# Performance work log

Hardware: AMD Instinct MI355X
Metric: run time of the kernel (lower is better)

The kernel has to match this reference:

```python
import jax, jax.numpy as jnp
import numpy as np

NEG_INF = -1e6  # d2l masked_softmax fill value


def setup_inputs() -> dict:
    key = jax.random.key(0)
    kq, kk, kv, kl = jax.random.split(key, 4)
    n, s, d = 32, 2048, 64
    queries = jax.random.normal(kq, (n, s, d), dtype=jnp.float32)
    keys = jax.random.normal(kk, (n, s, d), dtype=jnp.float32)
    values = jax.random.normal(kv, (n, s, d), dtype=jnp.float32)
    valid_lens = jax.random.randint(kl, (n,), 1, s + 1, dtype=jnp.int32)
    return {"queries": queries, "keys": keys, "values": values, "valid_lens": valid_lens}


def reference(queries, keys, values, valid_lens):
    d = queries.shape[-1]
    # scores: [n, q, k]
    scores = jnp.einsum("nqd,nkd->nqk", queries, keys) / jnp.sqrt(jnp.float32(d))
    kv_len = scores.shape[-1]
    # masked_softmax: positions >= valid_len get NEG_INF before softmax
    mask = jnp.arange(kv_len, dtype=jnp.int32)[None, None, :] < valid_lens[:, None, None]
    scores = jnp.where(mask, scores, NEG_INF)
    attn = jax.nn.softmax(scores, axis=-1)
    # dropout rate 0.0 (inference) -> identity
    return jnp.einsum("nqk,nkd->nqd", attn, values)
```

## Files before the change

### kernel.cpp

```cpp
#include <hip/hip_runtime.h>
#include <hip/hip_bf16.h>


typedef short bf16x8 __attribute__((ext_vector_type(8)));
typedef float f32x4  __attribute__((ext_vector_type(4)));
typedef float f32x16 __attribute__((ext_vector_type(16)));
typedef unsigned int u32;
typedef u32 u32x4 __attribute__((ext_vector_type(4)));

#define SEQ 2048
#define DH 64
#define BK 64
#define LDSP 72
#define FRAG 512
#define TILE_SH 4096
#define SCLQ 0.18033688011112042f

static __device__ __forceinline__ short f2bf(float f) {
    unsigned u = __float_as_uint(f);
    return (short)((u + 0x7FFFu + ((u >> 16) & 1u)) >> 16);
}
static __device__ __forceinline__ u32 pk2bf(float lo, float hi) {
    __hip_bfloat162 h = __float22bfloat162_rn(float2{lo, hi});
    return *(u32*)&h;
}
static __device__ __forceinline__ void pl32swap(u32& a, u32& b) {
    asm volatile("v_permlane32_swap_b32 %0, %1" : "+v"(a), "+v"(b));
}

__global__ __launch_bounds__(256, 4)
void prepass(const float* __restrict__ K, const float* __restrict__ V,
             short* __restrict__ KF, short* __restrict__ VF)
{
    __shared__ short T[DH][LDSP];

    const int tid  = threadIdx.x;
    const int wave = tid >> 6;
    const int lane = tid & 63;
    const int b  = blockIdx.x & 31;
    const int t  = blockIdx.x >> 5;
    const int k0 = t * BK;
    const size_t bo = (size_t)b * SEQ * DH;
    const size_t tb = (size_t)(b * 32 + t) * TILE_SH;

    const float* Ks = K + bo + (size_t)k0 * DH;
    short* Kd = KF + tb;
    #pragma unroll
    for (int h = 0; h < 2; ++h) {
        const int c = tid + h * 256;
        const int f = c >> 6;
        const int row = (f & 1) * 32 + (c & 31);
        const int col = (f >> 1) * 16 + ((c >> 5) & 1) * 8;
        f32x4 a = *(const f32x4*)(Ks + row * DH + col);
        f32x4 d = *(const f32x4*)(Ks + row * DH + col + 4);
        u32x4 o;
        o[0] = pk2bf(a[0], a[1]); o[1] = pk2bf(a[2], a[3]);
        o[2] = pk2bf(d[0], d[1]); o[3] = pk2bf(d[2], d[3]);
        *(u32x4*)(Kd + c * 8) = o;
    }

    #pragma unroll
    for (int h = 0; h < 2; ++h) {
        const int d0 = wave * 8 + h * 32;
        const float* src = V + bo + (size_t)(k0 + lane) * DH + d0;
        f32x4 va = *(const f32x4*)(src);
        f32x4 vb = *(const f32x4*)(src + 4);
        #pragma unroll
        for (int j = 0; j < 4; ++j) {
            T[d0 + j][lane]     = f2bf(va[j]);
            T[d0 + 4 + j][lane] = f2bf(vb[j]);
        }
    }
    __syncthreads();

    short* Vd = VF + tb;
    #pragma unroll
    for (int h = 0; h < 2; ++h) {
        const int c = tid + h * 256;
        const int f = c >> 6;
        const int trow = (f & 1) * 32 + (c & 31);
        const int tcol = (f >> 1) * 16 + ((c >> 5) & 1) * 8;
        *(bf16x8*)(Vd + c * 8) = *(const bf16x8*)(&T[trow][tcol]);
    }
}

template <bool PRE>
__global__ __launch_bounds__(256, 4)
void attn_fwd(const float* __restrict__ Q,
              const float* __restrict__ Kf, const float* __restrict__ Vf,
              const short* __restrict__ KF, const short* __restrict__ VF,
              const int* __restrict__ VL, float* __restrict__ O)
{
    __shared__ __align__(16) float Red[2][64][44];
    __shared__ int Rsort[32];

    const int tid  = threadIdx.x;
    const int wave = tid >> 6;
    const int lane = tid & 63;
    const int qg   = wave & 1;
    const int pg   = wave >> 1;
    const int hi   = lane >> 5;
    const int l31  = lane & 31;

    if (tid < 32) {
        const int nv = (VL[tid] + BK - 1) >> 6;
        int rank = 0;
        for (int jj = 0; jj < 32; ++jj) {
            const int nj = (VL[jj] + BK - 1) >> 6;
            rank += (nj > nv) || (nj == nv && jj < tid);
        }
        Rsort[rank] = tid;
    }
    __syncthreads();

    const int jb = blockIdx.x & 255;
    const int sl = blockIdx.x >> 8;
    const int c8 = jb >> 5;
    const int qt = jb & 31;
    const int rk = (sl == 0) ? c8 : (sl == 1) ? (15 - c8)
                 : (sl == 2) ? (16 + c8) : (31 - c8);
    int b = Rsort[rk];
    b = __builtin_amdgcn_readfirstlane(b);

    const int vl  = __builtin_amdgcn_readfirstlane(VL[b]);
    const int nkt = (vl + BK - 1) >> 6;

    const size_t bo = (size_t)b * SEQ * DH;
    const short* KFb = KF + (size_t)b * 32 * TILE_SH;
    const short* VFb = VF + (size_t)b * 32 * TILE_SH;
    const float* Kf32 = Kf + bo;
    const float* Vf32 = Vf + bo;

    const int qrow = qt * 64 + qg * 32 + l31;
    bf16x8 aq[4];
    {
        const float* qp = Q + bo + (size_t)qrow * DH + hi * 8;
        #pragma unroll
        for (int st = 0; st < 4; ++st) {
            f32x4 a = *(const f32x4*)(qp + st * 16);
            f32x4 c = *(const f32x4*)(qp + st * 16 + 4);
            #pragma unroll
            for (int j = 0; j < 4; ++j) {
                aq[st][j]     = f2bf(a[j] * SCLQ);
                aq[st][j + 4] = f2bf(c[j] * SCLQ);
            }
        }
    }

    f32x16 oacc0, oacc1;
    #pragma unroll
    for (int i = 0; i < 16; ++i) { oacc0[i] = 0.f; oacc1[i] = 0.f; }
    float Lrun = 0.f;

    const int lo8 = lane * 8;

    for (int kt = pg; kt < nkt; kt += 2) {
        const int k0 = kt * BK;
        const short* kf = KFb + (size_t)kt * TILE_SH;
        const short* vf = VFb + (size_t)kt * TILE_SH;

        auto ldA = [&](int f) -> bf16x8 {
            if constexpr (PRE) {
                return *(const bf16x8*)(kf + f * FRAG + lo8);
            } else {
                const int st = f >> 1, kh = f & 1;
                const float* p = Kf32 + (size_t)(k0 + kh * 32 + l31) * DH + st * 16 + hi * 8;
                f32x4 x = *(const f32x4*)p;
                f32x4 y = *(const f32x4*)(p + 4);
                bf16x8 r;
                #pragma unroll
                for (int j = 0; j < 4; ++j) { r[j] = f2bf(x[j]); r[j + 4] = f2bf(y[j]); }
                return r;
            }
        };
        auto ldV = [&](int f) -> bf16x8 {
            if constexpr (PRE) {
                return *(const bf16x8*)(vf + f * FRAG + lo8);
            } else {
                const int ks = f >> 1, dh = f & 1;
                bf16x8 r;
                #pragma unroll
                for (int j = 0; j < 8; ++j)
                    r[j] = f2bf(Vf32[(size_t)(k0 + ks * 16 + hi * 8 + j) * DH + dh * 32 + l31]);
                return r;
            }
        };

        f32x16 s0, s1;
        #pragma unroll
        for (int i = 0; i < 16; ++i) { s0[i] = 0.f; s1[i] = 0.f; }

        __builtin_amdgcn_s_setprio(1);
        bf16x8 A00 = ldA(0), A01 = ldA(1);
        bf16x8 A10 = ldA(2), A11 = ldA(3);
        s0 = __builtin_amdgcn_mfma_f32_32x32x16_bf16(A00, aq[0], s0, 0, 0, 0);
        s1 = __builtin_amdgcn_mfma_f32_32x32x16_bf16(A01, aq[0], s1, 0, 0, 0);
        bf16x8 A20 = ldA(4), A21 = ldA(5);
        s0 = __builtin_amdgcn_mfma_f32_32x32x16_bf16(A10, aq[1], s0, 0, 0, 0);
        s1 = __builtin_amdgcn_mfma_f32_32x32x16_bf16(A11, aq[1], s1, 0, 0, 0);
        bf16x8 A30 = ldA(6), A31 = ldA(7);
        s0 = __builtin_amdgcn_mfma_f32_32x32x16_bf16(A20, aq[2], s0, 0, 0, 0);
        s1 = __builtin_amdgcn_mfma_f32_32x32x16_bf16(A21, aq[2], s1, 0, 0, 0);
        s0 = __builtin_amdgcn_mfma_f32_32x32x16_bf16(A30, aq[3], s0, 0, 0, 0);
        s1 = __builtin_amdgcn_mfma_f32_32x32x16_bf16(A31, aq[3], s1, 0, 0, 0);
        __builtin_amdgcn_s_setprio(0);

        bf16x8 V00 = ldV(0), V01 = ldV(1);
        bf16x8 V10 = ldV(2), V11 = ldV(3);

        if (k0 + BK <= vl) {
            #pragma unroll
            for (int r = 0; r < 16; ++r) {
                s0[r] = __builtin_amdgcn_exp2f(s0[r]);
                s1[r] = __builtin_amdgcn_exp2f(s1[r]);
            }
        } else {
            #pragma unroll
            for (int r = 0; r < 16; ++r) {
                const int krow = k0 + (r & 3) + 8 * (r >> 2) + 4 * hi;
                s0[r] = (krow < vl)      ? __builtin_amdgcn_exp2f(s0[r]) : 0.f;
                s1[r] = (krow + 32 < vl) ? __builtin_amdgcn_exp2f(s1[r]) : 0.f;
            }
        }

        {
            float ls = 0.f;
            #pragma unroll
            for (int r = 0; r < 16; ++r) ls += s0[r] + s1[r];
            u32 a = __float_as_uint(ls), c = a;
            pl32swap(a, c);
            Lrun += __uint_as_float(a) + __uint_as_float(c);
        }

        u32 pk0[8], pk1[8];
        #pragma unroll
        for (int i = 0; i < 8; ++i) {
            pk0[i] = pk2bf(s0[2 * i], s0[2 * i + 1]);
            pk1[i] = pk2bf(s1[2 * i], s1[2 * i + 1]);
        }
        bf16x8 ap[4];
        #pragma unroll
        for (int t = 0; t < 2; ++t) {
            u32 x0 = pk0[4 * t], x1 = pk0[4 * t + 1];
            u32 x2 = pk0[4 * t + 2], x3 = pk0[4 * t + 3];
            pl32swap(x0, x2); pl32swap(x1, x3);
            u32x4 w; w[0] = x0; w[1] = x1; w[2] = x2; w[3] = x3;
            ap[t] = *(bf16x8*)&w;
            u32 y0 = pk1[4 * t], y1 = pk1[4 * t + 1];
            u32 y2 = pk1[4 * t + 2], y3 = pk1[4 * t + 3];
            pl32swap(y0, y2); pl32swap(y1, y3);
            u32x4 v; v[0] = y0; v[1] = y1; v[2] = y2; v[3] = y3;
            ap[2 + t] = *(bf16x8*)&v;
        }

        __builtin_amdgcn_s_setprio(1);
        oacc0 = __builtin_amdgcn_mfma_f32_32x32x16_bf16(ap[0], V00, oacc0, 0, 0, 0);
        oacc1 = __builtin_amdgcn_mfma_f32_32x32x16_bf16(ap[0], V01, oacc1, 0, 0, 0);
        bf16x8 V20 = ldV(4), V21 = ldV(5);
        oacc0 = __builtin_amdgcn_mfma_f32_32x32x16_bf16(ap[1], V10, oacc0, 0, 0, 0);
        oacc1 = __builtin_amdgcn_mfma_f32_32x32x16_bf16(ap[1], V11, oacc1, 0, 0, 0);
        bf16x8 V30 = ldV(6), V31 = ldV(7);
        oacc0 = __builtin_amdgcn_mfma_f32_32x32x16_bf16(ap[2], V20, oacc0, 0, 0, 0);
        oacc1 = __builtin_amdgcn_mfma_f32_32x32x16_bf16(ap[2], V21, oacc1, 0, 0, 0);
        oacc0 = __builtin_amdgcn_mfma_f32_32x32x16_bf16(ap[3], V30, oacc0, 0, 0, 0);
        oacc1 = __builtin_amdgcn_mfma_f32_32x32x16_bf16(ap[3], V31, oacc1, 0, 0, 0);
        __builtin_amdgcn_s_setprio(0);
    }

    float* rp = &Red[qg][lane][0];
    if (pg == 1) {
        #pragma unroll
        for (int wd = 0; wd < 4; ++wd) {
            f32x4 t0, t1;
            #pragma unroll
            for (int i = 0; i < 4; ++i) { t0[i] = oacc0[wd * 4 + i]; t1[i] = oacc1[wd * 4 + i]; }
            *(f32x4*)(rp + wd * 4)      = t0;
            *(f32x4*)(rp + 16 + wd * 4) = t1;
        }
        rp[32] = Lrun;
    }
    __syncthreads();
    if (pg == 0) {
        f32x4 p0[4], p1[4];
        #pragma unroll
        for (int wd = 0; wd < 4; ++wd) {
            p0[wd] = *(const f32x4*)(rp + wd * 4);
            p1[wd] = *(const f32x4*)(rp + 16 + wd * 4);
        }
        const float Lq = Lrun + rp[32];
        #pragma unroll
        for (int r = 0; r < 16; ++r) {
            const int rb = (r & 3) + 8 * (r >> 2) + 4 * hi;
            const float inv = 1.0f / __shfl(Lq, rb);
            const int row = qt * 64 + qg * 32 + rb;
            O[bo + (size_t)row * DH + l31]      = (oacc0[r] + p0[r >> 2][r & 3]) * inv;
            O[bo + (size_t)row * DH + 32 + l31] = (oacc1[r] + p1[r >> 2][r & 3]) * inv;
        }
    }
}

extern "C" void kernel_launch(void* const* d_in, const int* in_sizes, int n_in,
                              void* d_out, int out_size, void* d_ws, size_t ws_size,
                              hipStream_t stream) {
    const float* Q  = (const float*)d_in[0];
    const float* K  = (const float*)d_in[1];
    const float* V  = (const float*)d_in[2];
    const int*   VL = (const int*)d_in[3];
    float* O = (float*)d_out;

    const size_t nel = (size_t)32 * 32 * TILE_SH;
    const size_t need = 2 * nel * sizeof(short);
    if (ws_size >= need) {
        short* KF = (short*)d_ws;
        short* VF = KF + nel;
        prepass<<<dim3(1024), dim3(256), 0, stream>>>(K, V, KF, VF);
        attn_fwd<true><<<dim3(1024), dim3(256), 0, stream>>>(Q, K, V, KF, VF, VL, O);
    } else {
        attn_fwd<false><<<dim3(1024), dim3(256), 0, stream>>>(Q, K, V, nullptr, nullptr, VL, O);
    }
}
```

Baseline: 134.7 us.

## Split key tiles across four waves per 32-row query block with tree reduction

Each block now handles 32 query rows instead of 64, and all four waves stride over key tiles by four, so the grid doubles to 2048 blocks. Partial outputs and row sums are combined through a two-stage LDS tree reduction with an extra barrier. Block ordering becomes simple batch-rank-major, dropping the previous serpentine interleave. The aim is more parallelism and shorter per-wave key loops for the uneven valid lengths, at the cost of re-reading K/V tiles from twice as many blocks and extra reduction synchronisation.

```diff
diff --git a/kernel.cpp b/kernel.cpp
--- a/kernel.cpp
+++ b/kernel.cpp
@@ -14,6 +14,7 @@
 #define LDSP 72
 #define FRAG 512
 #define TILE_SH 4096
+#define PSTRIDE 36
 #define SCLQ 0.18033688011112042f
 
 static __device__ __forceinline__ short f2bf(float f) {
@@ -91,14 +92,12 @@
               const short* __restrict__ KF, const short* __restrict__ VF,
               const int* __restrict__ VL, float* __restrict__ O)
 {
-    __shared__ __align__(16) float Red[2][64][44];
+    __shared__ __align__(16) float Red[2][64][PSTRIDE];
     __shared__ int Rsort[32];
 
     const int tid  = threadIdx.x;
     const int wave = tid >> 6;
     const int lane = tid & 63;
-    const int qg   = wave & 1;
-    const int pg   = wave >> 1;
     const int hi   = lane >> 5;
     const int l31  = lane & 31;
 
@@ -113,12 +112,8 @@
     }
     __syncthreads();
 
-    const int jb = blockIdx.x & 255;
-    const int sl = blockIdx.x >> 8;
-    const int c8 = jb >> 5;
-    const int qt = jb & 31;
-    const int rk = (sl == 0) ? c8 : (sl == 1) ? (15 - c8)
-                 : (sl == 2) ? (16 + c8) : (31 - c8);
+    const int qq = blockIdx.x & 63;
+    const int rk = blockIdx.x >> 6;
     int b = Rsort[rk];
     b = __builtin_amdgcn_readfirstlane(b);
 
@@ -131,7 +126,7 @@
     const float* Kf32 = Kf + bo;
     const float* Vf32 = Vf + bo;
 
-    const int qrow = qt * 64 + qg * 32 + l31;
+    const int qrow = qq * 32 + l31;
     bf16x8 aq[4];
     {
         const float* qp = Q + bo + (size_t)qrow * DH + hi * 8;
@@ -154,7 +149,7 @@
 
     const int lo8 = lane * 8;
 
-    for (int kt = pg; kt < nkt; kt += 2) {
+    for (int kt = wave; kt < nkt; kt += 4) {
         const int k0 = kt * BK;
         const short* kf = KFb + (size_t)kt * TILE_SH;
         const short* vf = VFb + (size_t)kt * TILE_SH;
@@ -167,10 +162,10 @@
                 const float* p = Kf32 + (size_t)(k0 + kh * 32 + l31) * DH + st * 16 + hi * 8;
                 f32x4 x = *(const f32x4*)p;
                 f32x4 y = *(const f32x4*)(p + 4);
-                bf16x8 r;
+                bf16x8 rr;
                 #pragma unroll
-                for (int j = 0; j < 4; ++j) { r[j] = f2bf(x[j]); r[j + 4] = f2bf(y[j]); }
-                return r;
+                for (int j = 0; j < 4; ++j) { rr[j] = f2bf(x[j]); rr[j + 4] = f2bf(y[j]); }
+                return rr;
             }
         };
         auto ldV = [&](int f) -> bf16x8 {
@@ -178,11 +173,11 @@
                 return *(const bf16x8*)(vf + f * FRAG + lo8);
             } else {
                 const int ks = f >> 1, dh = f & 1;
-                bf16x8 r;
+                bf16x8 rr;
                 #pragma unroll
                 for (int j = 0; j < 8; ++j)
-                    r[j] = f2bf(Vf32[(size_t)(k0 + ks * 16 + hi * 8 + j) * DH + dh * 32 + l31]);
-                return r;
+                    rr[j] = f2bf(Vf32[(size_t)(k0 + ks * 16 + hi * 8 + j) * DH + dh * 32 + l31]);
+                return rr;
             }
         };
 
@@ -267,8 +262,8 @@
         __builtin_amdgcn_s_setprio(0);
     }
 
-    float* rp = &Red[qg][lane][0];
-    if (pg == 1) {
+    if (wave & 1) {
+        float* rp = &Red[wave >> 1][lane][0];
         #pragma unroll
         for (int wd = 0; wd < 4; ++wd) {
             f32x4 t0, t1;
@@ -280,21 +275,48 @@
         rp[32] = Lrun;
     }
     __syncthreads();
-    if (pg == 0) {
-        f32x4 p0[4], p1[4];
+    if (!(wave & 1)) {
+        const float* rp = &Red[wave >> 1][lane][0];
         #pragma unroll
         for (int wd = 0; wd < 4; ++wd) {
-            p0[wd] = *(const f32x4*)(rp + wd * 4);
-            p1[wd] = *(const f32x4*)(rp + 16 + wd * 4);
+            f32x4 t0 = *(const f32x4*)(rp + wd * 4);
+            f32x4 t1 = *(const f32x4*)(rp + 16 + wd * 4);
+            #pragma unroll
+            for (int i = 0; i < 4; ++i) { oacc0[wd * 4 + i] += t0[i]; oacc1[wd * 4 + i] += t1[i]; }
+        }
+        Lrun += rp[32];
+    }
+    __syncthreads();
+    if (wave == 2) {
+        float* rp = &Red[0][lane][0];
+        #pragma unroll
+        for (int wd = 0; wd < 4; ++wd) {
+            f32x4 t0, t1;
+            #pragma unroll
+            for (int i = 0; i < 4; ++i) { t0[i] = oacc0[wd * 4 + i]; t1[i] = oacc1[wd * 4 + i]; }
+            *(f32x4*)(rp + wd * 4)      = t0;
+            *(f32x4*)(rp + 16 + wd * 4) = t1;
+        }
+        rp[32] = Lrun;
+    }
+    __syncthreads();
+    if (wave == 0) {
+        const float* rp = &Red[0][lane][0];
+        #pragma unroll
+        for (int wd = 0; wd < 4; ++wd) {
+            f32x4 t0 = *(const f32x4*)(rp + wd * 4);
+            f32x4 t1 = *(const f32x4*)(rp + 16 + wd * 4);
+            #pragma unroll
+            for (int i = 0; i < 4; ++i) { oacc0[wd * 4 + i] += t0[i]; oacc1[wd * 4 + i] += t1[i]; }
         }
         const float Lq = Lrun + rp[32];
         #pragma unroll
         for (int r = 0; r < 16; ++r) {
             const int rb = (r & 3) + 8 * (r >> 2) + 4 * hi;
             const float inv = 1.0f / __shfl(Lq, rb);
-            const int row = qt * 64 + qg * 32 + rb;
-            O[bo + (size_t)row * DH + l31]      = (oacc0[r] + p0[r >> 2][r & 3]) * inv;
-            O[bo + (size_t)row * DH + 32 + l31] = (oacc1[r] + p1[r >> 2][r & 3]) * inv;
+            const int row = qq * 32 + rb;
+            O[bo + (size_t)row * DH + l31]      = oacc0[r] * inv;
+            O[bo + (size_t)row * DH + 32 + l31] = oacc1[r] * inv;
         }
     }
 }
@@ -308,14 +330,14 @@
     const int*   VL = (const int*)d_in[3];
     float* O = (float*)d_out;
 
-    const size_t nel = (size_t)32 * 32 * TILE_SH;
+    const size_t nel  = (size_t)32 * 32 * TILE_SH;
     const size_t need = 2 * nel * sizeof(short);
     if (ws_size >= need) {
         short* KF = (short*)d_ws;
         short* VF = KF + nel;
         prepass<<<dim3(1024), dim3(256), 0, stream>>>(K, V, KF, VF);
-        attn_fwd<true><<<dim3(1024), dim3(256), 0, stream>>>(Q, K, V, KF, VF, VL, O);
+        attn_fwd<true><<<dim3(2048), dim3(256), 0, stream>>>(Q, K, V, KF, VF, VL, O);
     } else {
-        attn_fwd<false><<<dim3(1024), dim3(256), 0, stream>>>(Q, K, V, nullptr, nullptr, VL, O);
-    }
-}
+        attn_fwd<false><<<dim3(2048), dim3(256), 0, stream>>>(Q, K, V, nullptr, nullptr, VL, O);
+    }
+}
```

After: 129.9 us. 1.04x faster.
